# Optimization experiments

Measured on AMD Instinct MI355X. Metric: run time of the kernel, lower is better.

Reference implementation:

```python
import jax, jax.numpy as jnp
import numpy as np

KERNEL = (2, 2, 2)  # kernel_shape == strides in the original module


def setup_inputs() -> dict:
    key = jax.random.key(0)
    x = jax.random.normal(key, (4, 32, 32, 32, 64), dtype=jnp.float32)
    return {"input_tensor": x}


def reference(input_tensor) -> jnp.ndarray:
    # conv3d_transpose with identity-at-corner kernel and stride==kernel_shape
    # places each input voxel at position (kd*d, kh*h, kw*w) of a zero output.
    b, d, h, w, c = input_tensor.shape
    kd, kh, kw = KERNEL
    out = jnp.zeros((b, d * kd, h * kh, w * kw, c), dtype=input_tensor.dtype)
    out = out.at[:, ::kd, ::kh, ::kw, :].set(input_tensor)
    return out
```

## Files before the change

kernel.cpp:

```cpp
#include <hip/hip_runtime.h>


#define UNROLL 8

typedef float f4 __attribute__((ext_vector_type(4)));

__global__ __launch_bounds__(256) void unpool3d_kernel(
    const f4* __restrict__ in, f4* __restrict__ out) {
    const int base = blockIdx.x * (256 * UNROLL) + threadIdx.x;
    f4 v[UNROLL];
#pragma unroll
    for (int k = 0; k < UNROLL; ++k) {
        const int i = base + k * 256;
        const int c4    = i & 15;
        const int voxel = i >> 4;
        const int wo = voxel & 63;
        const int ho = (voxel >> 6) & 63;
        const int dd = (voxel >> 12) & 63;
        const int b  = voxel >> 18;
        v[k] = (f4){0.f, 0.f, 0.f, 0.f};
        if (((wo | ho | dd) & 1) == 0) {
            const int in_voxel = ((b * 32 + (dd >> 1)) * 32 + (ho >> 1)) * 32 + (wo >> 1);
            v[k] = in[in_voxel * 16 + c4];
        }
    }
#pragma unroll
    for (int k = 0; k < UNROLL; ++k) {
        __builtin_nontemporal_store(v[k], &out[base + k * 256]);
    }
}

extern "C" void kernel_launch(void* const* d_in, const int* in_sizes, int n_in,
                              void* d_out, int out_size, void* d_ws, size_t ws_size,
                              hipStream_t stream) {
    const f4* in = (const f4*)d_in[0];
    f4* out = (f4*)d_out;
    const int n4 = out_size / 4;
    const int grid = n4 / (256 * UNROLL);
    unpool3d_kernel<<<grid, 256, 0, stream>>>(in, out);
}
```

Baseline: 52.24 us.

## Split unpooling into a zero-fill kernel and a linear-read scatter-copy kernel

The single fused kernel, which computed every output element and gathered input for even positions, is replaced by two launches. The first writes zeros only at non-corner output positions, using a bitmask on the linear index. The second reads the input contiguously and scatters each vector to its strided output location using bit-shift index remapping. The aim is fully coalesced input reads and simpler index arithmetic. The cost is a second kernel launch with no overlap between the two, and scattered writes from the copy kernel.

```diff
diff --git a/kernel.cpp b/kernel.cpp
--- a/kernel.cpp
+++ b/kernel.cpp
@@ -5,29 +5,33 @@
 
 typedef float f4 __attribute__((ext_vector_type(4)));
 
-__global__ __launch_bounds__(256) void unpool3d_kernel(
+__global__ __launch_bounds__(256) void unpool3d_zero_kernel(
+    f4* __restrict__ out) {
+    const int base = blockIdx.x * (256 * UNROLL) + threadIdx.x;
+    const f4 z = {0.f, 0.f, 0.f, 0.f};
+#pragma unroll
+    for (int k = 0; k < UNROLL; ++k) {
+        const int i = base + k * 256;
+        if ((i & 0x10410) != 0)
+            __builtin_nontemporal_store(z, &out[i]);
+    }
+}
+
+__global__ __launch_bounds__(256) void unpool3d_copy_kernel(
     const f4* __restrict__ in, f4* __restrict__ out) {
     const int base = blockIdx.x * (256 * UNROLL) + threadIdx.x;
     f4 v[UNROLL];
+    int oidx[UNROLL];
 #pragma unroll
     for (int k = 0; k < UNROLL; ++k) {
-        const int i = base + k * 256;
-        const int c4    = i & 15;
-        const int voxel = i >> 4;
-        const int wo = voxel & 63;
-        const int ho = (voxel >> 6) & 63;
-        const int dd = (voxel >> 12) & 63;
-        const int b  = voxel >> 18;
-        v[k] = (f4){0.f, 0.f, 0.f, 0.f};
-        if (((wo | ho | dd) & 1) == 0) {
-            const int in_voxel = ((b * 32 + (dd >> 1)) * 32 + (ho >> 1)) * 32 + (wo >> 1);
-            v[k] = in[in_voxel * 16 + c4];
-        }
+        const int g = base + k * 256;
+        v[k] = in[g];
+        oidx[k] = (g & 0xF) | ((g & 0x1F0) << 1) | ((g & 0x3E00) << 2)
+                | ((g & 0x1FC000) << 3);
     }
 #pragma unroll
-    for (int k = 0; k < UNROLL; ++k) {
-        __builtin_nontemporal_store(v[k], &out[base + k * 256]);
-    }
+    for (int k = 0; k < UNROLL; ++k)
+        __builtin_nontemporal_store(v[k], &out[oidx[k]]);
 }
 
 extern "C" void kernel_launch(void* const* d_in, const int* in_sizes, int n_in,
@@ -35,7 +39,10 @@
                               hipStream_t stream) {
     const f4* in = (const f4*)d_in[0];
     f4* out = (f4*)d_out;
-    const int n4 = out_size / 4;
-    const int grid = n4 / (256 * UNROLL);
-    unpool3d_kernel<<<grid, 256, 0, stream>>>(in, out);
+    const int n4_out = out_size / 4;
+    const int n4_in  = in_sizes[0] / 4;
+    const int gridA = n4_out / (256 * UNROLL);
+    const int gridB = n4_in  / (256 * UNROLL);
+    unpool3d_zero_kernel<<<gridA, 256, 0, stream>>>(out);
+    unpool3d_copy_kernel<<<gridB, 256, 0, stream>>>(in, out);
 }
```

Result: slower. 55.58 us (+6.4%).
